# Kernel optimization log

Measured on AMD Instinct MI355X. Metric: run time of the kernel, lower is better.

The kernel has to match this reference:

```python
import jax, jax.numpy as jnp
import numpy as np
from jax import lax

B, T, P, H, O = 64, 96, 256, 128, 24  # batch, seq_len, num_points, hidden_dim, pred_len


def setup_inputs() -> dict:
    key = jax.random.key(0)
    ks = jax.random.split(key, 7)
    s = 1.0 / np.sqrt(H)  # torch LSTM/Linear default init scale
    return {
        "x": jax.random.normal(ks[0], (B, T, P, 1), dtype=jnp.float32),
        "W_ih": jax.random.uniform(ks[1], (P, 4 * H, 1), jnp.float32, -s, s),
        "W_hh": jax.random.uniform(ks[2], (P, 4 * H, H), jnp.float32, -s, s),
        "b_ih": jax.random.uniform(ks[3], (P, 4 * H), jnp.float32, -s, s),
        "b_hh": jax.random.uniform(ks[4], (P, 4 * H), jnp.float32, -s, s),
        "W_fc": jax.random.uniform(ks[5], (P, O, H), jnp.float32, -s, s),
        "b_fc": jax.random.uniform(ks[6], (P, O), jnp.float32, -s, s),
    }


def reference(x, W_ih, W_hh, b_ih, b_hh, W_fc, b_fc):
    # x: [B, T, P, F]; model uses only feature 0
    xs = x[..., 0]  # [B, T, P]
    # input_dim == 1, so input-to-gate contribution is a scaled broadcast of W_ih
    # precompute for all timesteps: [T, B, P, 4H]
    gx = jnp.einsum("btp,pg->tbpg", xs, W_ih[:, :, 0]) + (b_ih + b_hh)

    def step(carry, gxt):
        h, c = carry  # [B, P, H] each
        gates = gxt + jnp.einsum("bph,pgh->bpg", h, W_hh)  # [B, P, 4H]
        i, f, g, o = jnp.split(gates, 4, axis=-1)  # torch gate order i,f,g,o
        i = jax.nn.sigmoid(i)
        f = jax.nn.sigmoid(f)
        g = jnp.tanh(g)
        o = jax.nn.sigmoid(o)
        c = f * c + i * g
        h = o * jnp.tanh(c)
        return (h, c), None

    h0 = jnp.zeros((B, P, H), dtype=x.dtype)
    (h, _), _ = lax.scan(step, (h0, h0), gx)
    # per-point Linear on final hidden state: [B, P, O]
    out = jnp.einsum("bph,poh->bpo", h, W_fc) + b_fc
    # original stacks point outputs on last dim -> [B, pred_len, P]
    return jnp.transpose(out, (0, 2, 1))
```

## Files before the change

### kernel.cpp

```cpp
#include <hip/hip_runtime.h>
#include <hip/hip_bf16.h>

#define Bdim 64
#define Tdim 96
#define Pdim 256
#define Hdim 128
#define Gdim 512
#define Odim 24
#define BH   32
#define WROW 132

typedef _Float16 f16x8 __attribute__((ext_vector_type(8)));
typedef float    f32x16 __attribute__((ext_vector_type(16)));
typedef float    f32x2  __attribute__((ext_vector_type(2)));

union H8 { uint2 u2[2]; unsigned short s[8]; _Float16 h[8]; f16x8 v; };
union HS { _Float16 h; unsigned short s; };

__device__ __forceinline__ float exp2_fast(float x) {
#if __has_builtin(__builtin_amdgcn_exp2f)
    return __builtin_amdgcn_exp2f(x);
#else
    return __expf(x * 0.6931471805599453f);
#endif
}

#define SGB __builtin_amdgcn_sched_group_barrier

__global__ __launch_bounds__(1024, 4)
void lstm_fused(const float* __restrict__ x,
                const float* __restrict__ W_ih,
                const float* __restrict__ W_hh,
                const float* __restrict__ b_ih,
                const float* __restrict__ b_hh,
                const float* __restrict__ W_fc,
                const float* __restrict__ b_fc,
                float* __restrict__ out)
{
    __shared__ unsigned short hb0[2][BH * WROW];
    __shared__ unsigned short hb1[2][BH * WROW];

    const int p   = blockIdx.x;
    const int tid = threadIdx.x;
    const int w   = tid >> 6;
    const int l31 = tid & 31;
    const int hi  = (tid >> 5) & 1;

    const float L1 = 1.4426950408889634f;
    const float L2 = 2.0f * L1;

    for (int i = tid; i < 2 * BH * WROW; i += 1024) {
        hb0[0][i < BH * WROW ? i : i - BH * WROW] = 0;
    }
    for (int i = tid; i < 2 * BH * WROW; i += 1024) {
        ((unsigned short*)hb0)[i] = 0;
    }
    for (int i = tid; i < 2 * BH * WROW; i += 1024) {
        ((unsigned short*)hb1)[i] = 0;
    }

    f16x8 afr[9];
    {
        const int rp   = w * 32 + l31;
        const int orow = ((rp & 3) << 7) | (rp >> 2);
        const float sc = ((rp & 3) == 2) ? L2 : L1;
        const float* rowp = W_hh + (size_t)p * Gdim * Hdim + (size_t)orow * Hdim;
        #pragma unroll
        for (int ks = 0; ks < 8; ++ks) {
            int k0 = ks * 16 + hi * 8;
            float4 va = *(const float4*)(rowp + k0);
            float4 vb = *(const float4*)(rowp + k0 + 4);
            H8 u;
            u.h[0] = (_Float16)(sc * va.x); u.h[1] = (_Float16)(sc * va.y);
            u.h[2] = (_Float16)(sc * va.z); u.h[3] = (_Float16)(sc * va.w);
            u.h[4] = (_Float16)(sc * vb.x); u.h[5] = (_Float16)(sc * vb.y);
            u.h[6] = (_Float16)(sc * vb.z); u.h[7] = (_Float16)(sc * vb.w);
            afr[ks] = u.v;
        }
        H8 u9;
        #pragma unroll
        for (int j = 0; j < 8; ++j) u9.s[j] = 0;
        if (hi == 0) {
            u9.h[0] = (_Float16)(sc * W_ih[(size_t)p * Gdim + orow]);
            u9.h[1] = (_Float16)(sc * (b_ih[(size_t)p * Gdim + orow] +
                                       b_hh[(size_t)p * Gdim + orow]));
        }
        afr[8] = u9.v;
    }

    const int lbase = l31 * (WROW * 2);

    auto ldh = [&](const char* hb, int ks) -> H8 {
        H8 r;
        int boff = lbase + ks * 32 + hi * 16;
        r.u2[0] = *(const uint2*)(hb + boff);
        r.u2[1] = *(const uint2*)(hb + boff + 8);
        return r;
    };

    auto ep_pair = [&](const f32x16& a, int j, f32x2* cr, unsigned short* wb) {
        f32x2 yi = {a[8 * j + 0], a[8 * j + 4]};
        f32x2 yf = {a[8 * j + 1], a[8 * j + 5]};
        f32x2 yg = {a[8 * j + 2], a[8 * j + 6]};
        f32x2 yo = {a[8 * j + 3], a[8 * j + 7]};
        f32x2 Ef = {exp2_fast(-yf.x), exp2_fast(-yf.y)};
        f32x2 Ei = {exp2_fast(-yi.x), exp2_fast(-yi.y)};
        f32x2 Eg = {exp2_fast(yg.x),  exp2_fast(yg.y)};
        f32x2 t1 = Ef + 1.0f;
        f32x2 t2 = Ei + 1.0f;
        f32x2 t3 = Eg + 1.0f;
        f32x2 t4 = Eg - 1.0f;
        f32x2 den = (t1 * t2) * t3;
        f32x2 num = (cr[j] * t2) * t3 + (L2 * t4) * t1;
        float D = den.x * den.y;
        float r = __builtin_amdgcn_rcpf(D);
        f32x2 inv = {r * den.y, r * den.x};
        f32x2 cn  = num * inv;
        cn.x = fminf(30.0f, fmaxf(-30.0f, cn.x));
        cn.y = fminf(30.0f, fmaxf(-30.0f, cn.y));
        cr[j] = cn;
        f32x2 Eo = {exp2_fast(-yo.x), exp2_fast(-yo.y)};
        f32x2 Ec = {exp2_fast(cn.x),  exp2_fast(cn.y)};
        f32x2 d2 = (Eo + 1.0f) * (Ec + 1.0f);
        float D2 = d2.x * d2.y;
        float r2 = __builtin_amdgcn_rcpf(D2);
        f32x2 j2 = {r2 * d2.y, r2 * d2.x};
        f32x2 hv = (Ec - 1.0f) * j2;
        HS ha; ha.h = (_Float16)hv.x;
        HS hc; hc.h = (_Float16)hv.y;
        int base = l31 * WROW + (w * 8 + 4 * j + hi);
        wb[base]     = ha.s;
        wb[base + 2] = hc.s;
    };

    auto phase = [&](const unsigned short* rb, unsigned short* wb,
                     f32x16& aw, const f32x16& ar, f32x2* cr, float xv,
                     bool doGemm, bool doEp) {
        if (doGemm) {
            const char* hb = (const char*)rb;
            H8 f0 = ldh(hb, 0), f1 = ldh(hb, 1);
            H8 f2 = ldh(hb, 2), f3 = ldh(hb, 3);
            f32x16 z;
            #pragma unroll
            for (int j = 0; j < 16; ++j) z[j] = 0.f;
            f32x16 a;
            a = __builtin_amdgcn_mfma_f32_32x32x16_f16(afr[0], f0.v, z, 0, 0, 0);
            a = __builtin_amdgcn_mfma_f32_32x32x16_f16(afr[1], f1.v, a, 0, 0, 0);
            if (doEp) ep_pair(ar, 0, cr, wb);
            H8 f4 = ldh(hb, 4), f5 = ldh(hb, 5);
            a = __builtin_amdgcn_mfma_f32_32x32x16_f16(afr[2], f2.v, a, 0, 0, 0);
            a = __builtin_amdgcn_mfma_f32_32x32x16_f16(afr[3], f3.v, a, 0, 0, 0);
            if (doEp) ep_pair(ar, 1, cr, wb);
            H8 f6 = ldh(hb, 6), f7 = ldh(hb, 7);
            a = __builtin_amdgcn_mfma_f32_32x32x16_f16(afr[4], f4.v, a, 0, 0, 0);
            a = __builtin_amdgcn_mfma_f32_32x32x16_f16(afr[5], f5.v, a, 0, 0, 0);
            a = __builtin_amdgcn_mfma_f32_32x32x16_f16(afr[6], f6.v, a, 0, 0, 0);
            a = __builtin_amdgcn_mfma_f32_32x32x16_f16(afr[7], f7.v, a, 0, 0, 0);
            H8 bg;
            #pragma unroll
            for (int j = 0; j < 8; ++j) bg.s[j] = 0;
            if (hi == 0) { bg.h[0] = (_Float16)xv; bg.h[1] = (_Float16)1.0f; }
            a = __builtin_amdgcn_mfma_f32_32x32x16_f16(afr[8], bg.v, a, 0, 0, 0);
            aw = a;
            if (doEp) {
                SGB(0x100, 2, 0);
                SGB(0x008, 1, 0);
                SGB(0x402, 25, 0);
                SGB(0x100, 2, 0);
                SGB(0x008, 1, 0);
                SGB(0x402, 25, 0);
                SGB(0x200, 2, 0);
                SGB(0x100, 2, 0);
                SGB(0x008, 2, 0);
                SGB(0x402, 25, 0);
                SGB(0x100, 2, 0);
                SGB(0x008, 2, 0);
                SGB(0x402, 25, 0);
                SGB(0x200, 2, 0);
                SGB(0x008, 3, 0);
            }
        } else if (doEp) {
            ep_pair(ar, 0, cr, wb);
            ep_pair(ar, 1, cr, wb);
        }
    };

    f32x2 cre0[2] = {f32x2{0.f, 0.f}, f32x2{0.f, 0.f}};
    f32x2 cre1[2] = {f32x2{0.f, 0.f}, f32x2{0.f, 0.f}};
    f32x16 acc0, acc1;
    #pragma unroll
    for (int j = 0; j < 16; ++j) { acc0[j] = 0.f; acc1[j] = 0.f; }

    const float* xp0 = x + (size_t)((0 * BH + l31) * Tdim) * Pdim + p;
    const float* xp1 = x + (size_t)((1 * BH + l31) * Tdim) * Pdim + p;
    float xv1 = xp1[0];

    __syncthreads();

    {
        float xv0 = xp0[0];
        phase(hb0[0], hb1[0], acc0, acc1, cre1, xv0, true, false);
    }
    __syncthreads();

    for (int t = 0; t < Tdim; ++t) {
        const int P  = t & 1;
        const int tn = (t + 1 < Tdim) ? (t + 1) : t;
        float xn0 = xp0[(size_t)tn * Pdim];

        phase(hb1[P], hb0[P ^ 1], acc1, acc0, cre0, xv1, true, true);
        __syncthreads();

        float xn1 = xp1[(size_t)tn * Pdim];
        if (t + 1 < Tdim) {
            phase(hb0[P ^ 1], hb1[P ^ 1], acc0, acc1, cre1, xn0, true, true);
        } else {
            phase(hb0[P ^ 1], hb1[P ^ 1], acc0, acc1, cre1, 0.f, false, true);
        }
        __syncthreads();
        xv1 = xn1;
    }

    const float* wfc = W_fc + (size_t)p * Odim * Hdim;
    const float* bfc = b_fc + (size_t)p * Odim;
    for (int i = tid; i < Bdim * Odim; i += 1024) {
        int o = i % Odim;
        int b = i / Odim;
        const unsigned short* hr = (b < BH) ? (hb0[0] + b * WROW)
                                            : (hb1[0] + (b - BH) * WROW);
        float s = bfc[o];
        const float* wr = wfc + o * Hdim;
        #pragma unroll 8
        for (int k2 = 0; k2 < Hdim; ++k2) {
            HS s2; s2.s = hr[k2];
            s = __builtin_fmaf(wr[k2], (float)s2.h, s);
        }
        out[(size_t)b * Odim * Pdim + (size_t)o * Pdim + p] = s;
    }
}

extern "C" void kernel_launch(void* const* d_in, const int* in_sizes, int n_in,
                              void* d_out, int out_size, void* d_ws, size_t ws_size,
                              hipStream_t stream) {
    const float* x    = (const float*)d_in[0];
    const float* W_ih = (const float*)d_in[1];
    const float* W_hh = (const float*)d_in[2];
    const float* b_ih = (const float*)d_in[3];
    const float* b_hh = (const float*)d_in[4];
    const float* W_fc = (const float*)d_in[5];
    const float* b_fc = (const float*)d_in[6];
    float* out = (float*)d_out;

    lstm_fused<<<dim3(Pdim), dim3(1024), 0, stream>>>(x, W_ih, W_hh, b_ih, b_hh, W_fc, b_fc, out);
}
```

Measured before the change: 399.2 us.

## Replace padded LDS hidden-state rows with XOR-swizzled layout and 128-bit reads

Replaces the padded hidden-state buffer (row stride 132) with an unpadded 128-element row layout where 16-byte chunks are XOR-swizzled by row index. The B-fragment load becomes a single 128-bit LDS read instead of two 64-bit reads, and writes and the final FC read use the matching swizzled index. It also removes the manual sched_group_barrier scheduling hints and uses fmed3 for the clamp. Dropping the hand-tuned schedule may let the compiler interleave MFMA and epilogue math less well, and the swizzle adds index arithmetic.

```diff
diff --git a/kernel.cpp b/kernel.cpp
--- a/kernel.cpp
+++ b/kernel.cpp
@@ -8,13 +8,12 @@
 #define Gdim 512
 #define Odim 24
 #define BH   32
-#define WROW 132
 
 typedef _Float16 f16x8 __attribute__((ext_vector_type(8)));
 typedef float    f32x16 __attribute__((ext_vector_type(16)));
 typedef float    f32x2  __attribute__((ext_vector_type(2)));
 
-union H8 { uint2 u2[2]; unsigned short s[8]; _Float16 h[8]; f16x8 v; };
+union H8 { uint4 u4; unsigned short s[8]; _Float16 h[8]; f16x8 v; };
 union HS { _Float16 h; unsigned short s; };
 
 __device__ __forceinline__ float exp2_fast(float x) {
@@ -24,8 +23,6 @@
     return __expf(x * 0.6931471805599453f);
 #endif
 }
-
-#define SGB __builtin_amdgcn_sched_group_barrier
 
 __global__ __launch_bounds__(1024, 4)
 void lstm_fused(const float* __restrict__ x,
@@ -37,8 +34,8 @@
                 const float* __restrict__ b_fc,
                 float* __restrict__ out)
 {
-    __shared__ unsigned short hb0[2][BH * WROW];
-    __shared__ unsigned short hb1[2][BH * WROW];
+    __shared__ unsigned short hb0[2][BH * Hdim];
+    __shared__ unsigned short hb1[2][BH * Hdim];
 
     const int p   = blockIdx.x;
     const int tid = threadIdx.x;
@@ -49,15 +46,8 @@
     const float L1 = 1.4426950408889634f;
     const float L2 = 2.0f * L1;
 
-    for (int i = tid; i < 2 * BH * WROW; i += 1024) {
-        hb0[0][i < BH * WROW ? i : i - BH * WROW] = 0;
-    }
-    for (int i = tid; i < 2 * BH * WROW; i += 1024) {
-        ((unsigned short*)hb0)[i] = 0;
-    }
-    for (int i = tid; i < 2 * BH * WROW; i += 1024) {
-        ((unsigned short*)hb1)[i] = 0;
-    }
+    for (int i = tid; i < 2 * BH * Hdim; i += 1024) ((unsigned short*)hb0)[i] = 0;
+    for (int i = tid; i < 2 * BH * Hdim; i += 1024) ((unsigned short*)hb1)[i] = 0;
 
     f16x8 afr[9];
     {
@@ -88,13 +78,11 @@
         afr[8] = u9.v;
     }
 
-    const int lbase = l31 * (WROW * 2);
-
-    auto ldh = [&](const char* hb, int ks) -> H8 {
+    auto ldh = [&](const unsigned short* hb, int ks) -> H8 {
         H8 r;
-        int boff = lbase + ks * 32 + hi * 16;
-        r.u2[0] = *(const uint2*)(hb + boff);
-        r.u2[1] = *(const uint2*)(hb + boff + 8);
+        int c   = ks * 2 + hi;
+        int off = (l31 << 8) + ((c ^ (l31 & 15)) << 4);
+        r.u4 = *(const uint4*)((const char*)hb + off);
         return r;
     };
 
@@ -116,8 +104,8 @@
         float r = __builtin_amdgcn_rcpf(D);
         f32x2 inv = {r * den.y, r * den.x};
         f32x2 cn  = num * inv;
-        cn.x = fminf(30.0f, fmaxf(-30.0f, cn.x));
-        cn.y = fminf(30.0f, fmaxf(-30.0f, cn.y));
+        cn.x = __builtin_amdgcn_fmed3f(cn.x, -30.0f, 30.0f);
+        cn.y = __builtin_amdgcn_fmed3f(cn.y, -30.0f, 30.0f);
         cr[j] = cn;
         f32x2 Eo = {exp2_fast(-yo.x), exp2_fast(-yo.y)};
         f32x2 Ec = {exp2_fast(cn.x),  exp2_fast(cn.y)};
@@ -128,57 +116,37 @@
         f32x2 hv = (Ec - 1.0f) * j2;
         HS ha; ha.h = (_Float16)hv.x;
         HS hc; hc.h = (_Float16)hv.y;
-        int base = l31 * WROW + (w * 8 + 4 * j + hi);
+        int base = (l31 << 7) + ((w ^ (l31 & 15)) << 3) + 4 * j + hi;
         wb[base]     = ha.s;
         wb[base + 2] = hc.s;
     };
 
     auto phase = [&](const unsigned short* rb, unsigned short* wb,
-                     f32x16& aw, const f32x16& ar, f32x2* cr, float xv,
+                     f32x16& acc, const f32x16& ar, f32x2* cr, float xv,
                      bool doGemm, bool doEp) {
         if (doGemm) {
-            const char* hb = (const char*)rb;
-            H8 f0 = ldh(hb, 0), f1 = ldh(hb, 1);
-            H8 f2 = ldh(hb, 2), f3 = ldh(hb, 3);
+            H8 f0 = ldh(rb, 0), f1 = ldh(rb, 1);
+            H8 f2 = ldh(rb, 2), f3 = ldh(rb, 3);
             f32x16 z;
             #pragma unroll
             for (int j = 0; j < 16; ++j) z[j] = 0.f;
-            f32x16 a;
-            a = __builtin_amdgcn_mfma_f32_32x32x16_f16(afr[0], f0.v, z, 0, 0, 0);
-            a = __builtin_amdgcn_mfma_f32_32x32x16_f16(afr[1], f1.v, a, 0, 0, 0);
+            acc = __builtin_amdgcn_mfma_f32_32x32x16_f16(afr[0], f0.v, z, 0, 0, 0);
+            acc = __builtin_amdgcn_mfma_f32_32x32x16_f16(afr[1], f1.v, acc, 0, 0, 0);
             if (doEp) ep_pair(ar, 0, cr, wb);
-            H8 f4 = ldh(hb, 4), f5 = ldh(hb, 5);
-            a = __builtin_amdgcn_mfma_f32_32x32x16_f16(afr[2], f2.v, a, 0, 0, 0);
-            a = __builtin_amdgcn_mfma_f32_32x32x16_f16(afr[3], f3.v, a, 0, 0, 0);
+            H8 f4 = ldh(rb, 4), f5 = ldh(rb, 5);
+            acc = __builtin_amdgcn_mfma_f32_32x32x16_f16(afr[2], f2.v, acc, 0, 0, 0);
+            acc = __builtin_amdgcn_mfma_f32_32x32x16_f16(afr[3], f3.v, acc, 0, 0, 0);
             if (doEp) ep_pair(ar, 1, cr, wb);
-            H8 f6 = ldh(hb, 6), f7 = ldh(hb, 7);
-            a = __builtin_amdgcn_mfma_f32_32x32x16_f16(afr[4], f4.v, a, 0, 0, 0);
-            a = __builtin_amdgcn_mfma_f32_32x32x16_f16(afr[5], f5.v, a, 0, 0, 0);
-            a = __builtin_amdgcn_mfma_f32_32x32x16_f16(afr[6], f6.v, a, 0, 0, 0);
-            a = __builtin_amdgcn_mfma_f32_32x32x16_f16(afr[7], f7.v, a, 0, 0, 0);
+            H8 f6 = ldh(rb, 6), f7 = ldh(rb, 7);
+            acc = __builtin_amdgcn_mfma_f32_32x32x16_f16(afr[4], f4.v, acc, 0, 0, 0);
+            acc = __builtin_amdgcn_mfma_f32_32x32x16_f16(afr[5], f5.v, acc, 0, 0, 0);
+            acc = __builtin_amdgcn_mfma_f32_32x32x16_f16(afr[6], f6.v, acc, 0, 0, 0);
+            acc = __builtin_amdgcn_mfma_f32_32x32x16_f16(afr[7], f7.v, acc, 0, 0, 0);
             H8 bg;
             #pragma unroll
             for (int j = 0; j < 8; ++j) bg.s[j] = 0;
             if (hi == 0) { bg.h[0] = (_Float16)xv; bg.h[1] = (_Float16)1.0f; }
-            a = __builtin_amdgcn_mfma_f32_32x32x16_f16(afr[8], bg.v, a, 0, 0, 0);
-            aw = a;
-            if (doEp) {
-                SGB(0x100, 2, 0);
-                SGB(0x008, 1, 0);
-                SGB(0x402, 25, 0);
-                SGB(0x100, 2, 0);
-                SGB(0x008, 1, 0);
-                SGB(0x402, 25, 0);
-                SGB(0x200, 2, 0);
-                SGB(0x100, 2, 0);
-                SGB(0x008, 2, 0);
-                SGB(0x402, 25, 0);
-                SGB(0x100, 2, 0);
-                SGB(0x008, 2, 0);
-                SGB(0x402, 25, 0);
-                SGB(0x200, 2, 0);
-                SGB(0x008, 3, 0);
-            }
+            acc = __builtin_amdgcn_mfma_f32_32x32x16_f16(afr[8], bg.v, acc, 0, 0, 0);
         } else if (doEp) {
             ep_pair(ar, 0, cr, wb);
             ep_pair(ar, 1, cr, wb);
@@ -226,13 +194,15 @@
     for (int i = tid; i < Bdim * Odim; i += 1024) {
         int o = i % Odim;
         int b = i / Odim;
-        const unsigned short* hr = (b < BH) ? (hb0[0] + b * WROW)
-                                            : (hb1[0] + (b - BH) * WROW);
+        int bl = (b < BH) ? b : (b - BH);
+        const unsigned short* hr = (b < BH) ? (hb0[0] + (bl << 7))
+                                            : (hb1[0] + (bl << 7));
         float s = bfc[o];
         const float* wr = wfc + o * Hdim;
         #pragma unroll 8
         for (int k2 = 0; k2 < Hdim; ++k2) {
-            HS s2; s2.s = hr[k2];
+            int idx = (((k2 >> 3) ^ (bl & 15)) << 3) + (k2 & 7);
+            HS s2; s2.s = hr[idx];
             s = __builtin_fmaf(wr[k2], (float)s2.h, s);
         }
         out[(size_t)b * Odim * Pdim + (size_t)o * Pdim + p] = s;
```

New measurement: 390.9 us. 2.1% less time.
